# Performance work log

Measured on AMD Instinct MI355X. Metric: run time of the kernel, lower is better.

The kernel has to match this reference:

```python
import jax, jax.numpy as jnp
import numpy as np

N_NODES = 300000
N_EDGES = 1200000
D = 128
B = 1000
VOCAB = 26  # vocab_size + 1


def setup_inputs() -> dict:
    key = jax.random.key(0)
    ks = jax.random.split(key, 10)
    x = jax.random.randint(ks[0], (N_NODES,), 0, VOCAB, dtype=jnp.int32)
    edge_index = jax.random.randint(ks[1], (2, N_EDGES), 0, N_NODES, dtype=jnp.int32)
    # cumulative protein boundaries: B proteins of equal length, last entry == N_NODES
    amino_acids_numbers = (jnp.arange(1, B + 1, dtype=jnp.int32) * (N_NODES // B))
    s = 1.0 / np.sqrt(D)
    emb = jax.random.normal(ks[2], (VOCAB, D), dtype=jnp.float32)
    W_rel1 = jax.random.uniform(ks[3], (D, D), jnp.float32, -s, s)
    b_rel1 = jax.random.uniform(ks[4], (D,), jnp.float32, -s, s)
    W_root1 = jax.random.uniform(ks[5], (D, D), jnp.float32, -s, s)
    W_rel2 = jax.random.uniform(ks[6], (D, D), jnp.float32, -s, s)
    b_rel2 = jax.random.uniform(ks[7], (D,), jnp.float32, -s, s)
    W_root2 = jax.random.uniform(ks[8], (D, D), jnp.float32, -s, s)
    return {"x": x, "edge_index": edge_index, "amino_acids_numbers": amino_acids_numbers,
            "emb": emb, "W_rel1": W_rel1, "b_rel1": b_rel1, "W_root1": W_root1,
            "W_rel2": W_rel2, "b_rel2": b_rel2, "W_root2": W_root2}


def _graph_conv(nodes, src, tgt, W_rel, b_rel, W_root, n):
    # PyG GraphConv (aggr='add'): out = Lin_rel(sum_{j->i} x_j) + Lin_root(x_i)
    agg = jax.ops.segment_sum(nodes[src], tgt, num_segments=n)  # [N, D]
    return agg @ W_rel.T + b_rel + nodes @ W_root.T


def reference(x, edge_index, amino_acids_numbers, emb,
              W_rel1, b_rel1, W_root1, W_rel2, b_rel2, W_root2):
    n = x.shape[0]
    src, tgt = edge_index[0], edge_index[1]
    nodes = emb[x]  # [N, D] embedding lookup
    nodes = _graph_conv(nodes, src, tgt, W_rel1, b_rel1, W_root1, n)
    nodes = _graph_conv(nodes, src, tgt, W_rel2, b_rel2, W_root2, n)
    # segment mean pooling over [start:end) slices defined by cumulative ends
    ends = amino_acids_numbers
    seg = jnp.searchsorted(ends, jnp.arange(n), side='right')  # node -> protein id
    b = ends.shape[0]
    sums = jax.ops.segment_sum(nodes, seg, num_segments=b)  # [B, D]
    counts = jnp.diff(ends, prepend=jnp.zeros((1,), ends.dtype)).astype(nodes.dtype)
    return sums / counts[:, None]
```

## Files before the change

### kernel.cpp

```cpp
#include <hip/hip_runtime.h>

#define DD 128
#define VV 26
#define NW 13
#define CS4 4
#define G 256
#define TWIN 512
#define PAD 4096

__device__ __forceinline__ unsigned wsum(unsigned v) {
#pragma unroll
    for (int m = 32; m >= 1; m >>= 1) v += __shfl_xor(v, m, 64);
    return v;
}

__device__ __forceinline__ int wscan_incl(int v) {
    int lane = threadIdx.x & 63;
#pragma unroll
    for (int off = 1; off < 64; off <<= 1) {
        int t = __shfl_up(v, off, 64);
        if (lane >= off) v += t;
    }
    return v;
}

__device__ __forceinline__ int seg_guess(const int* ends, int B, int t, int Lavg) {
    int p = t / Lavg;
    if (p > B - 1) p = B - 1;
    while (p > 0 && ends[p - 1] > t) --p;
    while (ends[p] <= t) ++p;
    return p;
}

__device__ __forceinline__ int bseg(const int* cumx, int j) {
    int lo = 0, hi = G - 1;
    while (lo < hi) {
        int mid = (lo + hi + 1) >> 1;
        if (cumx[mid] <= j) lo = mid; else hi = mid - 1;
    }
    return lo;
}

__global__ __launch_bounds__(1024)
void k_sort_pre(const int* __restrict__ src, const int* __restrict__ tgt,
                const int* __restrict__ x, const int* __restrict__ ends,
                int E, int B, int chunk, int Lavg,
                const float* __restrict__ emb,
                const float* __restrict__ W1r, const float* __restrict__ b1,
                const float* __restrict__ W1o,
                const float* __restrict__ W2r, const float* __restrict__ W2o,
                unsigned long long* __restrict__ sorted_ts,
                int* __restrict__ segstartT, int* __restrict__ seghistT,
                float* __restrict__ P1, float* __restrict__ P2,
                float* __restrict__ P3, float* __restrict__ uvec,
                float* __restrict__ wvec) {
    extern __shared__ char smem[];
    int tid = threadIdx.x;
    int chunkp = (chunk + 1) & ~1;

    if (blockIdx.x >= G) {
        float* e1r = (float*)smem;
        float* r1r = e1r + DD;
        float* b1s = r1r + DD;
        int v = blockIdx.x - G;
        int d = tid;
        if (d < DD) {
            const float* e = emb + v * DD;
            const float* w1r = W1r + d * DD;
            const float* w1o = W1o + d * DD;
            float s1 = 0.f, s2 = 0.f;
            for (int k = 0; k < DD; ++k) { float ev = e[k]; s1 += ev * w1r[k]; s2 += ev * w1o[k]; }
            e1r[d] = s1; r1r[d] = s2; b1s[d] = b1[d];
        }
        __syncthreads();
        if (d < DD) {
            const float* wr = W2r + d * DD;
            const float* wo = W2o + d * DD;
            float p1 = 0.f, p2 = 0.f, p3 = 0.f, su = 0.f, sw = 0.f;
            for (int k = 0; k < DD; ++k) {
                float a = wr[k], bb = wo[k], ee = e1r[k], r = r1r[k], c = b1s[k];
                p1 += ee * a; p2 += r * a + ee * bb; p3 += r * bb;
                su += c * a; sw += c * bb;
            }
            P1[v * DD + d] = p1; P2[v * DD + d] = p2; P3[v * DD + d] = p3;
            if (v == 0) { uvec[d] = su; wvec[d] = sw; }
        }
        return;
    }

    int* lds_ends = (int*)smem;
    int* hist = lds_ends + 1024;
    int* cur = hist + 1024;
    int* wsums = cur + 1024;
    unsigned short* lpe = (unsigned short*)(wsums + 16);

    int b = blockIdx.x;
    int e0 = b * chunk;
    int e1 = min(E, e0 + chunk);
    int clen = e1 - e0;

    for (int i = tid; i < B; i += 1024) lds_ends[i] = ends[i];
    hist[tid] = 0;
    __syncthreads();

    for (int i = tid; i < clen; i += 1024) {
        int t = tgt[e0 + i];
        int p = seg_guess(lds_ends, B, t, Lavg);
        atomicAdd(&hist[p], 1);
        lpe[i] = (unsigned short)p;
    }
    __syncthreads();

    int v = hist[tid];
    if (tid < B) seghistT[tid * G + b] = v;
    int wave = tid >> 6, lane = tid & 63;
    int incl = wscan_incl(v);
    if (lane == 63) wsums[wave] = incl;
    __syncthreads();
    int offw = 0;
    for (int w = 0; w < wave; ++w) offw += wsums[w];
    int excl = incl + offw - v;
    if (tid < B) {
        cur[tid] = excl;
        segstartT[tid * G + b] = e0 + excl;
    }
    __syncthreads();

    for (int i = tid; i < clen; i += 1024) {
        int e = e0 + i;
        int p = lpe[i];
        int s = src[e];
        int t = tgt[e];
        int lbl = x[s];
        int pst = (p == 0) ? 0 : lds_ends[p - 1];
        int pos = atomicAdd(&cur[p], 1);
        sorted_ts[e0 + pos] = ((unsigned long long)(unsigned)s << 16)
                            | (unsigned long long)(unsigned)(((t - pst) << 5) | lbl);
    }
}

__global__ __launch_bounds__(256)
void k_counts(const int* __restrict__ ends,
              const int* __restrict__ seghistT, const int* __restrict__ segstartT,
              int B, int E, const unsigned long long* __restrict__ sorted_ts,
              unsigned* __restrict__ counts, unsigned* __restrict__ csG,
              int* __restrict__ DpG, float* __restrict__ CpG) {
    __shared__ unsigned tab[TWIN * CS4];
    __shared__ int cumx[G + 4], segb[G], wsums[4];
    __shared__ unsigned red[4][16];
    int p = blockIdx.x, tid = threadIdx.x;
    int wave = tid >> 6, lane = tid & 63;
    int start = (p == 0) ? 0 : ends[p - 1];
    int end = ends[p];
    int Lp = end - start;

    int h = seghistT[p * G + tid];
    segb[tid] = segstartT[p * G + tid];
    int incl = wscan_incl(h);
    if (lane == 63) wsums[wave] = incl;
    __syncthreads();
    int offw = 0;
    for (int w = 0; w < wave; ++w) offw += wsums[w];
    cumx[tid] = incl + offw - h;
    if (tid == 255) { cumx[G] = incl + offw; DpG[p] = incl + offw; }
    __syncthreads();
    int Dp = cumx[G];

    unsigned cp[16];
#pragma unroll
    for (int k = 0; k < 16; ++k) cp[k] = 0u;

    for (int w0 = 0; w0 < Lp; w0 += TWIN) {
        int wlen = min(TWIN, Lp - w0);
        __syncthreads();
        for (int i = tid; i < wlen * CS4; i += 256) tab[i] = 0u;
        __syncthreads();
        for (int j = tid; j < Dp; j += 256) {
            int bb = bseg(cumx, j);
            int pos = segb[bb] + (j - cumx[bb]);
            unsigned long long ts = sorted_ts[pos];
            unsigned tl = (unsigned)(ts & 0xFFFFull);
            if (w0 == 0) csG[(size_t)p * PAD + j] = (unsigned)(ts >> 16);
            int lbl = (int)(tl & 31u);
            int tloc = (int)(tl >> 5) - w0;
            if ((unsigned)tloc < (unsigned)wlen)
                atomicAdd(&tab[tloc * CS4 + (lbl >> 3)], 1u << ((lbl & 7) * 4));
        }
        __syncthreads();
        unsigned* dst = counts + ((size_t)(start + w0)) * CS4;
        for (int i = tid; i < wlen * CS4; i += 256) dst[i] = tab[i];
        for (int r = tid; r < wlen; r += 256) {
            uint4 c0 = *reinterpret_cast<const uint4*>(&tab[r * CS4]);
            unsigned w;
            w = c0.x; cp[0]  += w & 0x000F000Fu; cp[1]  += (w >> 4) & 0x000F000Fu;
                      cp[2]  += (w >> 8) & 0x000F000Fu; cp[3]  += (w >> 12) & 0x000F000Fu;
            w = c0.y; cp[4]  += w & 0x000F000Fu; cp[5]  += (w >> 4) & 0x000F000Fu;
                      cp[6]  += (w >> 8) & 0x000F000Fu; cp[7]  += (w >> 12) & 0x000F000Fu;
            w = c0.z; cp[8]  += w & 0x000F000Fu; cp[9]  += (w >> 4) & 0x000F000Fu;
                      cp[10] += (w >> 8) & 0x000F000Fu; cp[11] += (w >> 12) & 0x000F000Fu;
            w = c0.w; cp[12] += w & 0x000F000Fu; cp[13] += (w >> 4) & 0x000F000Fu;
                      cp[14] += (w >> 8) & 0x000F000Fu; cp[15] += (w >> 12) & 0x000F000Fu;
        }
    }

#pragma unroll
    for (int k = 0; k < 16; ++k) {
        unsigned a = wsum(cp[k]); if (lane == 0) red[wave][k] = a;
    }
    __syncthreads();
    if (tid < 16) {
        unsigned t = red[0][tid] + red[1][tid] + red[2][tid] + red[3][tid];
        int base = 8 * (tid >> 2) + (tid & 3);
        if (base < VV) CpG[(size_t)p * VV + base] = (float)(t & 0xFFFFu);
        if (base + 4 < VV) CpG[(size_t)p * VV + base + 4] = (float)(t >> 16);
    }
}

__global__ __launch_bounds__(256)
void k_protein(const int* __restrict__ x, const int* __restrict__ ends,
               const int* __restrict__ DpG, const unsigned* __restrict__ csG,
               const unsigned* __restrict__ counts, const float* __restrict__ CpG,
               const float* __restrict__ P1, const float* __restrict__ P2,
               const float* __restrict__ P3, const float* __restrict__ uvec,
               const float* __restrict__ wvec, const float* __restrict__ b2,
               int B, int E, float* __restrict__ out) {
    __shared__ unsigned red[4][32];
    __shared__ float c2f[VV], cpf[VV], hpf[VV];
    int p = blockIdx.x, tid = threadIdx.x;
    int wave = tid >> 6, lane = tid & 63;
    int start = (p == 0) ? 0 : ends[p - 1];
    int end = ends[p];
    int Dp = DpG[p];

    if (tid < VV) cpf[tid] = CpG[(size_t)p * VV + tid];

    unsigned c2[16], hpw[NW];
#pragma unroll
    for (int k = 0; k < 16; ++k) c2[k] = 0u;
#pragma unroll
    for (int w = 0; w < NW; ++w) hpw[w] = 0u;

    const unsigned* cs = csG + (size_t)p * PAD;
    for (int j = tid; j < Dp; j += 256) {
        int s = (int)cs[j];
        uint4 c0 = *reinterpret_cast<const uint4*>(counts + (size_t)s * CS4);
        unsigned w;
        w = c0.x; c2[0]  += w & 0x000F000Fu; c2[1]  += (w >> 4) & 0x000F000Fu;
                  c2[2]  += (w >> 8) & 0x000F000Fu; c2[3]  += (w >> 12) & 0x000F000Fu;
        w = c0.y; c2[4]  += w & 0x000F000Fu; c2[5]  += (w >> 4) & 0x000F000Fu;
                  c2[6]  += (w >> 8) & 0x000F000Fu; c2[7]  += (w >> 12) & 0x000F000Fu;
        w = c0.z; c2[8]  += w & 0x000F000Fu; c2[9]  += (w >> 4) & 0x000F000Fu;
                  c2[10] += (w >> 8) & 0x000F000Fu; c2[11] += (w >> 12) & 0x000F000Fu;
        w = c0.w; c2[12] += w & 0x000F000Fu; c2[13] += (w >> 4) & 0x000F000Fu;
                  c2[14] += (w >> 8) & 0x000F000Fu; c2[15] += (w >> 12) & 0x000F000Fu;
    }

    for (int i = start + tid; i < end; i += 256) {
        int l = x[i];
        unsigned inc = 1u << ((l & 1) * 16);
        int wi = l >> 1;
#pragma unroll
        for (int w2 = 0; w2 < NW; ++w2) hpw[w2] += (w2 == wi) ? inc : 0u;
    }

#pragma unroll
    for (int k = 0; k < 16; ++k) {
        unsigned a = wsum(c2[k]); if (lane == 0) red[wave][k] = a;
    }
#pragma unroll
    for (int w = 0; w < NW; ++w) {
        unsigned a = wsum(hpw[w]); if (lane == 0) red[wave][16 + w] = a;
    }
    __syncthreads();
    if (tid < 16 + NW) {
        unsigned t = red[0][tid] + red[1][tid] + red[2][tid] + red[3][tid];
        if (tid < 16) {
            int base = 8 * (tid >> 2) + (tid & 3);
            if (base < VV) c2f[base] = (float)(t & 0xFFFFu);
            if (base + 4 < VV) c2f[base + 4] = (float)(t >> 16);
        } else {
            int w = tid - 16;
            hpf[w * 2] = (float)(t & 0xFFFFu);
            if (w * 2 + 1 < VV) hpf[w * 2 + 1] = (float)(t >> 16);
        }
    }
    __syncthreads();

    if (tid < DD) {
        int d = tid;
        float acc = 0.f;
#pragma unroll
        for (int v = 0; v < VV; ++v)
            acc += c2f[v] * P1[v * DD + d] + cpf[v] * P2[v * DD + d] + hpf[v] * P3[v * DD + d];
        float Lp = (float)(end - start);
        float invL = 1.f / Lp;
        float Dpf = (float)Dp;
        out[(size_t)p * DD + d] = acc * invL + (Dpf * invL) * uvec[d] + wvec[d] + b2[d];
    }
}

extern "C" void kernel_launch(void* const* d_in, const int* in_sizes, int n_in,
                              void* d_out, int out_size, void* d_ws, size_t ws_size,
                              hipStream_t stream) {
    const int*   x       = (const int*)d_in[0];
    const int*   edge    = (const int*)d_in[1];
    const int*   ends    = (const int*)d_in[2];
    const float* emb     = (const float*)d_in[3];
    const float* W_rel1  = (const float*)d_in[4];
    const float* b_rel1  = (const float*)d_in[5];
    const float* W_root1 = (const float*)d_in[6];
    const float* W_rel2  = (const float*)d_in[7];
    const float* b_rel2  = (const float*)d_in[8];
    const float* W_root2 = (const float*)d_in[9];

    const int N = in_sizes[0];
    const int E = in_sizes[1] / 2;
    const int B = in_sizes[2];
    const int Lavg = (N / B) > 0 ? (N / B) : 1;
    const int chunk = (E + G - 1) / G;
    const int chunkp = (chunk + 1) & ~1;

    const int* srcp = edge;
    const int* tgtp = edge + E;

    auto align256 = [](size_t v) { return (v + 255) & ~(size_t)255; };
    char* ws = (char*)d_ws;
    size_t off = 0;
    unsigned* counts = (unsigned*)(ws + off);                 off += align256((size_t)N * CS4 * 4);
    int* segstartT = (int*)(ws + off);                        off += align256((size_t)B * G * 4);
    int* seghistT = (int*)(ws + off);                         off += align256((size_t)B * G * 4);
    int* DpG = (int*)(ws + off);                              off += align256((size_t)B * 4);
    unsigned long long* sorted_ts = (unsigned long long*)(ws + off); off += align256((size_t)E * 8);
    unsigned* csG = (unsigned*)(ws + off);                    off += align256((size_t)B * PAD * 4);
    float* CpG = (float*)(ws + off);                          off += align256((size_t)B * VV * 4);
    float* P1 = (float*)(ws + off);                           off += align256((size_t)VV * DD * 4);
    float* P2 = (float*)(ws + off);                           off += align256((size_t)VV * DD * 4);
    float* P3 = (float*)(ws + off);                           off += align256((size_t)VV * DD * 4);
    float* uvec = (float*)(ws + off);                         off += align256((size_t)DD * 4);
    float* wvec = (float*)(ws + off);                         off += align256((size_t)DD * 4);
    (void)ws_size; (void)n_in; (void)out_size;


    size_t ldsb = (size_t)(3 * 1024 + 16) * 4 + (size_t)chunkp * 2;
    k_sort_pre<<<G + VV, 1024, ldsb, stream>>>(
        srcp, tgtp, x, ends, E, B, chunk, Lavg,
        emb, W_rel1, b_rel1, W_root1, W_rel2, W_root2,
        sorted_ts, segstartT, seghistT, P1, P2, P3, uvec, wvec);

    k_counts<<<B, 256, 0, stream>>>(ends, seghistT, segstartT, B, E, sorted_ts,
                                    counts, csG, DpG, CpG);

    k_protein<<<B, 256, 0, stream>>>(x, ends, DpG, csG, counts, CpG,
                                     P1, P2, P3, uvec, wvec, b_rel2, B, E, (float*)d_out);
}
```

Before: 69.12 us.

## Pack sorted edges into 32-bit keys, stage in LDS, defer label lookup

The sorted edge payload shrinks from 64-bit to 32-bit (local target shifted by 19 bits over a 19-bit source index). Sorted entries are now staged in LDS and written out to global memory with coalesced stores instead of scattered ones. The x[s] label gather moves from the sort kernel into the counts kernel, where it runs only for edges inside the current target window. This cuts global traffic and scatter cost, but assumes N fits in 19 bits and per-protein local target indices fit in 13 bits, and it re-gathers x once per window pass.

```diff
diff --git a/kernel.cpp b/kernel.cpp
--- a/kernel.cpp
+++ b/kernel.cpp
@@ -7,6 +7,7 @@
 #define G 256
 #define TWIN 512
 #define PAD 4096
+#define SBITS 19
 
 __device__ __forceinline__ unsigned wsum(unsigned v) {
 #pragma unroll
@@ -43,13 +44,13 @@
 
 __global__ __launch_bounds__(1024)
 void k_sort_pre(const int* __restrict__ src, const int* __restrict__ tgt,
-                const int* __restrict__ x, const int* __restrict__ ends,
+                const int* __restrict__ ends,
                 int E, int B, int chunk, int Lavg,
                 const float* __restrict__ emb,
                 const float* __restrict__ W1r, const float* __restrict__ b1,
                 const float* __restrict__ W1o,
                 const float* __restrict__ W2r, const float* __restrict__ W2o,
-                unsigned long long* __restrict__ sorted_ts,
+                unsigned* __restrict__ sorted_ts,
                 int* __restrict__ segstartT, int* __restrict__ seghistT,
                 float* __restrict__ P1, float* __restrict__ P2,
                 float* __restrict__ P3, float* __restrict__ uvec,
@@ -88,7 +89,8 @@
         return;
     }
 
-    int* lds_ends = (int*)smem;
+    unsigned* pay = (unsigned*)smem;
+    int* lds_ends = (int*)(pay + chunk);
     int* hist = lds_ends + 1024;
     int* cur = hist + 1024;
     int* wsums = cur + 1024;
@@ -131,18 +133,19 @@
         int p = lpe[i];
         int s = src[e];
         int t = tgt[e];
-        int lbl = x[s];
         int pst = (p == 0) ? 0 : lds_ends[p - 1];
         int pos = atomicAdd(&cur[p], 1);
-        sorted_ts[e0 + pos] = ((unsigned long long)(unsigned)s << 16)
-                            | (unsigned long long)(unsigned)(((t - pst) << 5) | lbl);
-    }
+        pay[pos] = ((unsigned)(t - pst) << SBITS) | (unsigned)s;
+    }
+    __syncthreads();
+
+    for (int i = tid; i < clen; i += 1024) sorted_ts[e0 + i] = pay[i];
 }
 
 __global__ __launch_bounds__(256)
-void k_counts(const int* __restrict__ ends,
+void k_counts(const int* __restrict__ x, const int* __restrict__ ends,
               const int* __restrict__ seghistT, const int* __restrict__ segstartT,
-              int B, int E, const unsigned long long* __restrict__ sorted_ts,
+              int B, int E, const unsigned* __restrict__ sorted_ts,
               unsigned* __restrict__ counts, unsigned* __restrict__ csG,
               int* __restrict__ DpG, float* __restrict__ CpG) {
     __shared__ unsigned tab[TWIN * CS4];
@@ -178,13 +181,14 @@
         for (int j = tid; j < Dp; j += 256) {
             int bb = bseg(cumx, j);
             int pos = segb[bb] + (j - cumx[bb]);
-            unsigned long long ts = sorted_ts[pos];
-            unsigned tl = (unsigned)(ts & 0xFFFFull);
-            if (w0 == 0) csG[(size_t)p * PAD + j] = (unsigned)(ts >> 16);
-            int lbl = (int)(tl & 31u);
-            int tloc = (int)(tl >> 5) - w0;
-            if ((unsigned)tloc < (unsigned)wlen)
+            unsigned ts = sorted_ts[pos];
+            int s = (int)(ts & ((1u << SBITS) - 1u));
+            int tloc = (int)(ts >> SBITS) - w0;
+            if (w0 == 0) csG[(size_t)p * PAD + j] = (unsigned)s;
+            if ((unsigned)tloc < (unsigned)wlen) {
+                int lbl = x[s];
                 atomicAdd(&tab[tloc * CS4 + (lbl >> 3)], 1u << ((lbl & 7) * 4));
+            }
         }
         __syncthreads();
         unsigned* dst = counts + ((size_t)(start + w0)) * CS4;
@@ -330,7 +334,7 @@
     int* segstartT = (int*)(ws + off);                        off += align256((size_t)B * G * 4);
     int* seghistT = (int*)(ws + off);                         off += align256((size_t)B * G * 4);
     int* DpG = (int*)(ws + off);                              off += align256((size_t)B * 4);
-    unsigned long long* sorted_ts = (unsigned long long*)(ws + off); off += align256((size_t)E * 8);
+    unsigned* sorted_ts = (unsigned*)(ws + off);              off += align256((size_t)E * 4);
     unsigned* csG = (unsigned*)(ws + off);                    off += align256((size_t)B * PAD * 4);
     float* CpG = (float*)(ws + off);                          off += align256((size_t)B * VV * 4);
     float* P1 = (float*)(ws + off);                           off += align256((size_t)VV * DD * 4);
@@ -341,13 +345,13 @@
     (void)ws_size; (void)n_in; (void)out_size;
 
 
-    size_t ldsb = (size_t)(3 * 1024 + 16) * 4 + (size_t)chunkp * 2;
+    size_t ldsb = (size_t)chunk * 4 + (size_t)(3 * 1024 + 16) * 4 + (size_t)chunkp * 2;
     k_sort_pre<<<G + VV, 1024, ldsb, stream>>>(
-        srcp, tgtp, x, ends, E, B, chunk, Lavg,
+        srcp, tgtp, ends, E, B, chunk, Lavg,
         emb, W_rel1, b_rel1, W_root1, W_rel2, W_root2,
         sorted_ts, segstartT, seghistT, P1, P2, P3, uvec, wvec);
 
-    k_counts<<<B, 256, 0, stream>>>(ends, seghistT, segstartT, B, E, sorted_ts,
+    k_counts<<<B, 256, 0, stream>>>(x, ends, seghistT, segstartT, B, E, sorted_ts,
                                     counts, csG, DpG, CpG);
 
     k_protein<<<B, 256, 0, stream>>>(x, ends, DpG, csG, counts, CpG,
```

New measurement: 60.27 us. -12.8%, faster.
